# Kernel optimization log

Measured on AMD Instinct MI355X. Metric: run time of the kernel, lower is better.

## Reference

```python
import jax, jax.numpy as jnp
import numpy as np

NV = 100000   # vehicle nodes
NE = 100000   # 'edge' nodes (dst type)
E = 250000    # graph edges (connects relation)
VDIM = 16
EDIM = 16
HID = 128
HEADS = 4
DH = 128      # out_feats per head (GATv2Conv(hid, hid))
EPS = 1e-5
NEG_SLOPE = 0.2


def _layernorm(x, g, b):
    mu = x.mean(-1, keepdims=True)
    var = ((x - mu) ** 2).mean(-1, keepdims=True)
    return (x - mu) * jax.lax.rsqrt(var + EPS) * g + b


def setup_inputs() -> dict:
    key = jax.random.key(0)
    ks = jax.random.split(key, 20)
    s = 0.05
    return {
        "v_feat": jax.random.normal(ks[0], (NV, VDIM), jnp.float32),
        "e_feat": jax.random.normal(ks[1], (NE, EDIM), jnp.float32),
        "Wv": jax.random.normal(ks[2], (VDIM, HID), jnp.float32) * s,
        "bv": jnp.zeros((HID,), jnp.float32),
        "gv": jnp.ones((HID,), jnp.float32),
        "betav": jnp.zeros((HID,), jnp.float32),
        "We": jax.random.normal(ks[3], (EDIM, HID), jnp.float32) * s,
        "be": jnp.zeros((HID,), jnp.float32),
        "ge": jnp.ones((HID,), jnp.float32),
        "betae": jnp.zeros((HID,), jnp.float32),
        "Wsrc": jax.random.normal(ks[4], (HID, HEADS * DH), jnp.float32) * s,
        "bsrc": jnp.zeros((HEADS * DH,), jnp.float32),
        "Wdst": jax.random.normal(ks[5], (HID, HEADS * DH), jnp.float32) * s,
        "bdst": jnp.zeros((HEADS * DH,), jnp.float32),
        "attn": jax.random.normal(ks[6], (HEADS, DH), jnp.float32) * s,
        "Wp": jax.random.normal(ks[7], (HID, HID), jnp.float32) * s,
        "bp": jnp.zeros((HID,), jnp.float32),
        "src": jax.random.randint(ks[8], (E,), 0, NV, jnp.int32),
        "dst": jax.random.randint(ks[9], (E,), 0, NE, jnp.int32),
    }


def reference(v_feat, e_feat, Wv, bv, gv, betav, We, be, ge, betae,
              Wsrc, bsrc, Wdst, bdst, attn, Wp, bp, src, dst):
    # --- node-type encoders: Linear -> ReLU -> LayerNorm ---
    h_v = _layernorm(jax.nn.relu(v_feat @ Wv + bv), gv, betav)      # [NV, HID]
    h_e = _layernorm(jax.nn.relu(e_feat @ We + be), ge, betae)      # [NE, HID]

    # --- GATv2Conv (bipartite: vehicle -> edge), 4 heads ---
    fs = (h_v @ Wsrc + bsrc).reshape(NV, HEADS, DH)                 # src proj
    fd = (h_e @ Wdst + bdst).reshape(NE, HEADS, DH)                 # dst proj
    e = jax.nn.leaky_relu(fs[src] + fd[dst], NEG_SLOPE)             # [E, H, D]
    score = jnp.einsum("ehd,hd->eh", e, attn)                       # [E, H]
    # segment-wise (per-dst-node) softmax over incoming edges
    smax = jax.ops.segment_max(score, dst, num_segments=NE)         # [NE, H]
    ex = jnp.exp(score - smax[dst])
    denom = jax.ops.segment_sum(ex, dst, num_segments=NE)
    alpha = ex / denom[dst]                                         # [E, H]
    out = jax.ops.segment_sum(alpha[:, :, None] * fs[src], dst,
                              num_segments=NE)                      # [NE, H, D]

    # HeteroGraphConv mean-aggregate (single relation -> identity),
    # then mean over heads (edge_out.dim()==3 branch)
    edge_out = out.mean(axis=1)                                     # [NE, HID]

    # feature_proj: Linear -> ReLU -> Dropout(eval: identity)
    return jax.nn.relu(edge_out @ Wp + bp)
```

## Files before the change

### kernel.cpp

```cpp
#include <hip/hip_runtime.h>
#include <hip/hip_bf16.h>
#include <math.h>

#define NV 100000
#define NE_N 100000
#define NEDGE 250000
#define NPAD 100032
#define NEG 0.2f
#define LN_EPS 1e-5f

typedef __bf16 bf16_t;
typedef __bf16 bf16x8 __attribute__((ext_vector_type(8)));
typedef float f32x4 __attribute__((ext_vector_type(4)));
typedef float f32x2 __attribute__((ext_vector_type(2)));

__device__ inline unsigned short f2bfu(float f) {
    return __builtin_bit_cast(unsigned short, (__bf16)f);
}
__device__ inline float blo(unsigned w) { return __uint_as_float(w << 16); }
__device__ inline float bhi(unsigned w) { return __uint_as_float(w & 0xffff0000u); }
__device__ inline float lrelu(float x) { return x > 0.f ? x : NEG * x; }
__device__ inline unsigned pk2(float a, float b) {
    return (unsigned)f2bfu(a) | ((unsigned)f2bfu(b) << 16);
}

__device__ __forceinline__ void gload_lds16(const void* g, void* l) {
    __builtin_amdgcn_global_load_lds(
        (const __attribute__((address_space(1))) unsigned int*)g,
        (__attribute__((address_space(3))) unsigned int*)l,
        16, 0, 0);
}

__global__ __launch_bounds__(256) void prep_kernel(
    const float* __restrict__ Wsrc, const float* __restrict__ Wdst,
    const float* __restrict__ Wp, bf16_t* __restrict__ pS,
    bf16_t* __restrict__ pD, bf16_t* __restrict__ pP,
    int* __restrict__ deg, int* __restrict__ gctr)
{
    int t = blockIdx.x * 256 + threadIdx.x;
    if (t == 0) *gctr = 0;
    if (t < 8192) {
        int ksq = t >> 9, col = t & 511;
#pragma unroll
        for (int j = 0; j < 8; ++j)
            pS[(size_t)t * 8 + j] = (bf16_t)Wsrc[(ksq * 8 + j) * 512 + col];
    } else if (t < 16384) {
        int g = t - 8192;
        int ksq = g >> 9, col = g & 511;
#pragma unroll
        for (int j = 0; j < 8; ++j)
            pD[(size_t)g * 8 + j] = (bf16_t)Wdst[(ksq * 8 + j) * 512 + col];
    } else if (t < 18432) {
        int g = t - 16384;
        int ksq = g >> 7, col = g & 127;
#pragma unroll
        for (int j = 0; j < 8; ++j)
            pP[(size_t)g * 8 + j] = (bf16_t)Wp[(ksq * 8 + j) * 128 + col];
    } else {
        int z = t - 18432;
        if (z < NE_N) deg[z] = 0;
    }
}

__global__ __launch_bounds__(256) void count_kernel(
    const int* __restrict__ dst, int* __restrict__ deg)
{
    int t = blockIdx.x * 256 + threadIdx.x;
    if (t < NEDGE) atomicAdd(&deg[dst[t]], 1);
}

__global__ __launch_bounds__(256) void reserve_kernel(
    const int* __restrict__ deg, int* __restrict__ cursor,
    int2* __restrict__ od, int* __restrict__ gctr)
{
    __shared__ int s[256];
    __shared__ int base;
    int i = blockIdx.x * 256 + threadIdx.x;
    int v = (i < NE_N) ? deg[i] : 0;
    s[threadIdx.x] = v;
    __syncthreads();
    for (int off = 1; off < 256; off <<= 1) {
        int t_ = (threadIdx.x >= off) ? s[threadIdx.x - off] : 0;
        __syncthreads();
        s[threadIdx.x] += t_;
        __syncthreads();
    }
    if (threadIdx.x == 255) base = atomicAdd(gctr, s[255]);
    __syncthreads();
    if (i < NE_N) {
        int o = base + s[threadIdx.x] - v;
        cursor[i] = o;
        od[i] = make_int2(o, v);
    }
}

__global__ __launch_bounds__(256) void scatter_kernel(
    const int* __restrict__ dst, const int* __restrict__ src,
    int* __restrict__ cursor, int* __restrict__ srcs)
{
    int t = blockIdx.x * 256 + threadIdx.x;
    if (t < NEDGE) {
        int pos = atomicAdd(&cursor[dst[t]], 1);
        srcs[pos] = src[t];
    }
}

__global__ __launch_bounds__(256, 4) void enc_proj_kernel(
    const float* __restrict__ featV, const float* __restrict__ WencV,
    const float* __restrict__ bencV, const float* __restrict__ gV,
    const float* __restrict__ betaV, const bf16_t* __restrict__ ApackV,
    const float* __restrict__ bprojV, unsigned short* __restrict__ outV,
    const float* __restrict__ featE, const float* __restrict__ WencE,
    const float* __restrict__ bencE, const float* __restrict__ gE,
    const float* __restrict__ betaE, const bf16_t* __restrict__ ApackE,
    const float* __restrict__ bprojE, unsigned short* __restrict__ outE,
    int nblk1, int M)
{
    __shared__ unsigned short Hs[64 * 136];
    __shared__ __align__(16) unsigned short Abuf[2][8192];
    __shared__ __align__(16) float Bias[512];

    int b = blockIdx.x;
    bool isV = b < nblk1;
    const float* feat  = isV ? featV  : featE;
    const float* Wenc  = isV ? WencV  : WencE;
    const float* benc  = isV ? bencV  : bencE;
    const float* gln   = isV ? gV     : gE;
    const float* beta  = isV ? betaV  : betaE;
    const bf16_t* Apack = isV ? ApackV : ApackE;
    const float* bproj = isV ? bprojV : bprojE;
    unsigned short* out = isV ? outV : outE;
    int row0 = (isV ? b : b - nblk1) * 64;

    int t = threadIdx.x;
    int l = t & 63;
    int w = t >> 6;
    int rbase = __builtin_amdgcn_readfirstlane(w * 16);

    {
        int sr = row0 + rbase + (l >> 2);
        if (sr > M - 1) sr = M - 1;
        gload_lds16(feat + (size_t)sr * 16 + (l & 3) * 4, &Abuf[1][w * 512]);
    }

#pragma unroll
    for (int j = 0; j < 4; ++j) {
        int ksq = w * 4 + j;
        gload_lds16(Apack + ((size_t)(ksq * 512) + l) * 8, &Abuf[0][ksq * 512]);
    }
    if (t < 128)
        *(float4*)&Bias[t * 4] = *(const float4*)(bproj + t * 4);

    f32x2 wc2[16];
#pragma unroll
    for (int k = 0; k < 16; ++k) {
        float2 wv = *(const float2*)(Wenc + k * 128 + 2 * l);
        wc2[k][0] = wv.x;
        wc2[k][1] = wv.y;
    }
    float2 bv2 = *(const float2*)(benc + 2 * l);

    asm volatile("s_waitcnt vmcnt(0)" ::: "memory");

    const float* Fs = (const float*)&Abuf[1][0];
#pragma unroll
    for (int i = 0; i < 16; ++i) {
        const float* fr = Fs + (rbase + i) * 16;
        float4 f0 = *(const float4*)(fr);
        float4 f1 = *(const float4*)(fr + 4);
        float4 f2 = *(const float4*)(fr + 8);
        float4 f3 = *(const float4*)(fr + 12);
        f32x2 a = {bv2.x, bv2.y};
        a = __builtin_elementwise_fma((f32x2)f0.x, wc2[0],  a);
        a = __builtin_elementwise_fma((f32x2)f0.y, wc2[1],  a);
        a = __builtin_elementwise_fma((f32x2)f0.z, wc2[2],  a);
        a = __builtin_elementwise_fma((f32x2)f0.w, wc2[3],  a);
        a = __builtin_elementwise_fma((f32x2)f1.x, wc2[4],  a);
        a = __builtin_elementwise_fma((f32x2)f1.y, wc2[5],  a);
        a = __builtin_elementwise_fma((f32x2)f1.z, wc2[6],  a);
        a = __builtin_elementwise_fma((f32x2)f1.w, wc2[7],  a);
        a = __builtin_elementwise_fma((f32x2)f2.x, wc2[8],  a);
        a = __builtin_elementwise_fma((f32x2)f2.y, wc2[9],  a);
        a = __builtin_elementwise_fma((f32x2)f2.z, wc2[10], a);
        a = __builtin_elementwise_fma((f32x2)f2.w, wc2[11], a);
        a = __builtin_elementwise_fma((f32x2)f3.x, wc2[12], a);
        a = __builtin_elementwise_fma((f32x2)f3.y, wc2[13], a);
        a = __builtin_elementwise_fma((f32x2)f3.z, wc2[14], a);
        a = __builtin_elementwise_fma((f32x2)f3.w, wc2[15], a);
        float a0 = fmaxf(a[0], 0.f);
        float a1 = fmaxf(a[1], 0.f);
        *(unsigned*)&Hs[(rbase + i) * 136 + 2 * l] = pk2(a0, a1);
    }

    float s = 0.f, s2 = 0.f;
    {
        int rr = rbase + (l >> 2);
        int q = l & 3;
#pragma unroll
        for (int j = 0; j < 4; ++j) {
            uint4 v = *(const uint4*)&Hs[rr * 136 + q * 32 + j * 8];
            float x;
            x = blo(v.x); s += x; s2 = fmaf(x, x, s2);
            x = bhi(v.x); s += x; s2 = fmaf(x, x, s2);
            x = blo(v.y); s += x; s2 = fmaf(x, x, s2);
            x = bhi(v.y); s += x; s2 = fmaf(x, x, s2);
            x = blo(v.z); s += x; s2 = fmaf(x, x, s2);
            x = bhi(v.z); s += x; s2 = fmaf(x, x, s2);
            x = blo(v.w); s += x; s2 = fmaf(x, x, s2);
            x = bhi(v.w); s += x; s2 = fmaf(x, x, s2);
        }
    }
    s  += __shfl_xor(s, 1, 64);  s  += __shfl_xor(s, 2, 64);
    s2 += __shfl_xor(s2, 1, 64); s2 += __shfl_xor(s2, 2, 64);
    float mu  = s * (1.f / 128.f);
    float var = s2 * (1.f / 128.f) - mu * mu;
    float inv = rsqrtf(var + LN_EPS);

    int kq = l >> 4;
    int ln = l & 15;
    float mu_r  = __shfl(mu,  ln * 4, 64);
    float inv_r = __shfl(inv, ln * 4, 64);

    bf16x8 bfr[4];
#pragma unroll
    for (int ks = 0; ks < 4; ++ks) {
        int c0 = ks * 32 + kq * 8;
        uint4 v = *(const uint4*)&Hs[(rbase + ln) * 136 + c0];
        float4 g0 = *(const float4*)(gln + c0);
        float4 g1 = *(const float4*)(gln + c0 + 4);
        float4 b0 = *(const float4*)(beta + c0);
        float4 b1 = *(const float4*)(beta + c0 + 4);
        uint4 p;
        p.x = pk2(fmaf((blo(v.x) - mu_r) * inv_r, g0.x, b0.x),
                  fmaf((bhi(v.x) - mu_r) * inv_r, g0.y, b0.y));
        p.y = pk2(fmaf((blo(v.y) - mu_r) * inv_r, g0.z, b0.z),
                  fmaf((bhi(v.y) - mu_r) * inv_r, g0.w, b0.w));
        p.z = pk2(fmaf((blo(v.z) - mu_r) * inv_r, g1.x, b1.x),
                  fmaf((bhi(v.z) - mu_r) * inv_r, g1.y, b1.y));
        p.w = pk2(fmaf((blo(v.w) - mu_r) * inv_r, g1.z, b1.z),
                  fmaf((bhi(v.w) - mu_r) * inv_r, g1.w, b1.w));
        bfr[ks] = __builtin_bit_cast(bf16x8, p);
    }

    unsigned short* stag = Hs + rbase * 136;
    int node = row0 + rbase + ln;

#pragma unroll
    for (int p = 0; p < 8; ++p) {
        if (p == 0)
            asm volatile("s_waitcnt lgkmcnt(0)" ::: "memory");
        else
            asm volatile("s_waitcnt vmcnt(2)" ::: "memory");
        __builtin_amdgcn_s_barrier();

        if (p < 7) {
#pragma unroll
            for (int j = 0; j < 4; ++j) {
                int ksq = w * 4 + j;
                gload_lds16(Apack + ((size_t)(ksq * 512 + (p + 1) * 64) + l) * 8,
                            &Abuf[(p + 1) & 1][ksq * 512]);
            }
            __builtin_amdgcn_sched_barrier(0);
        }

        const unsigned short* Ac = Abuf[p & 1];
#pragma unroll
        for (int mt = 0; mt < 4; ++mt) {
            bf16x8 a[4];
#pragma unroll
            for (int ks = 0; ks < 4; ++ks)
                a[ks] = *(const bf16x8*)&Ac[((ks * 4 + kq) * 64 + mt * 16 + ln) * 8];

            f32x4 acc = {0.f, 0.f, 0.f, 0.f};
#pragma unroll
            for (int ks = 0; ks < 4; ++ks)
                acc = __builtin_amdgcn_mfma_f32_16x16x32_bf16(a[ks], bfr[ks], acc, 0, 0, 0);

            int colp = p * 64 + mt * 16 + kq * 4;
            float4 bb = *(const float4*)&Bias[colp];
            ushort4 o;
            o.x = f2bfu(acc[0] + bb.x);
            o.y = f2bfu(acc[1] + bb.y);
            o.z = f2bfu(acc[2] + bb.z);
            o.w = f2bfu(acc[3] + bb.w);
            *(ushort4*)&stag[ln * 136 + mt * 16 + kq * 4] = o;
        }
#pragma unroll
        for (int i = 0; i < 2; ++i) {
            uint4 v = *(const uint4*)&stag[ln * 136 + i * 32 + kq * 8];
            *(uint4*)(out + (size_t)node * 512 + p * 64 + i * 32 + kq * 8) = v;
        }
    }
}

__global__ __launch_bounds__(256) void final_gemm_kernel(
    const float* __restrict__ A, const unsigned short* __restrict__ Abf,
    const bf16_t* __restrict__ Ppack, const float* __restrict__ bp,
    float* __restrict__ C, int M)
{
    __shared__ unsigned short Hs[64 * 136];
    int t = threadIdx.x;
    int lane = t & 63;
    int w = t >> 6;
    int row0 = blockIdx.x * 64;

    if (Abf) {
#pragma unroll
        for (int i = 0; i < 4; ++i) {
            int idx = i * 256 + t;
            int r = idx >> 4;
            int c = (idx & 15) * 8;
            uint4 v = make_uint4(0, 0, 0, 0);
            if (row0 + r < M)
                v = *(const uint4*)(Abf + (size_t)(row0 + r) * 128 + c);
            *(uint4*)&Hs[r * 136 + c] = v;
        }
    } else {
#pragma unroll
        for (int i = 0; i < 8; ++i) {
            int f4 = i * 256 + t;
            int r = f4 >> 5;
            int c4 = (f4 & 31) * 4;
            float4 v = make_float4(0.f, 0.f, 0.f, 0.f);
            if (row0 + r < M)
                v = ((const float4*)(A + (size_t)(row0 + r) * 128))[f4 & 31];
            ushort4 o;
            o.x = f2bfu(v.x); o.y = f2bfu(v.y); o.z = f2bfu(v.z); o.w = f2bfu(v.w);
            *(ushort4*)&Hs[r * 136 + c4] = o;
        }
    }
    __syncthreads();

    int kq = lane >> 4;
    int ln = lane & 15;

    f32x4 acc[2][4];
#pragma unroll
    for (int mt = 0; mt < 2; ++mt)
#pragma unroll
        for (int nt = 0; nt < 4; ++nt) {
            f32x4 z = {0.f, 0.f, 0.f, 0.f};
            acc[mt][nt] = z;
        }

#pragma unroll
    for (int ks = 0; ks < 4; ++ks) {
        bf16x8 bfr[4];
#pragma unroll
        for (int nt = 0; nt < 4; ++nt) {
            const uint4* p = (const uint4*)&Hs[(nt * 16 + ln) * 136 + ks * 32 + kq * 8];
            bfr[nt] = __builtin_bit_cast(bf16x8, *p);
        }
        bf16x8 afr[2];
#pragma unroll
        for (int mt = 0; mt < 2; ++mt) {
            int colA = w * 32 + mt * 16 + ln;
            afr[mt] = *(const bf16x8*)(Ppack + ((size_t)(ks * 4 + kq) * 128 + colA) * 8);
        }
#pragma unroll
        for (int mt = 0; mt < 2; ++mt)
#pragma unroll
            for (int nt = 0; nt < 4; ++nt)
                acc[mt][nt] = __builtin_amdgcn_mfma_f32_16x16x32_bf16(
                    afr[mt], bfr[nt], acc[mt][nt], 0, 0, 0);
    }

#pragma unroll
    for (int mt = 0; mt < 2; ++mt) {
        int col = w * 32 + mt * 16 + kq * 4;
        float4 bb = *(const float4*)(bp + col);
#pragma unroll
        for (int nt = 0; nt < 4; ++nt) {
            int node = row0 + nt * 16 + ln;
            if (node < M) {
                float4 o;
                o.x = fmaxf(acc[mt][nt][0] + bb.x, 0.f);
                o.y = fmaxf(acc[mt][nt][1] + bb.y, 0.f);
                o.z = fmaxf(acc[mt][nt][2] + bb.z, 0.f);
                o.w = fmaxf(acc[mt][nt][3] + bb.w, 0.f);
                *(float4*)(C + (size_t)node * 128 + col) = o;
            }
        }
    }
}

__global__ __launch_bounds__(256) void softagg_kernel(
    const unsigned short* __restrict__ fs, const unsigned short* __restrict__ fdp,
    const float* __restrict__ attn, const int2* __restrict__ od,
    const int* __restrict__ srcs, float* __restrict__ outf,
    unsigned short* __restrict__ eo)
{
    __shared__ __align__(16) unsigned short Ebuf[4][4][512];
    int wq = threadIdx.x >> 6;
    int d = blockIdx.x * 4 + wq;
    if (d >= NE_N) return;
    int l = threadIdx.x & 63;
    int2 rd = od[d];
    int r0 = rd.x;
    int n  = rd.y;
    int o = l * 8;

    uint4 fv = *(const uint4*)(fdp + (size_t)d * 512 + o);
    float fdv[8] = { blo(fv.x), bhi(fv.x), blo(fv.y), bhi(fv.y),
                     blo(fv.z), bhi(fv.z), blo(fv.w), bhi(fv.w) };
    float4 w0 = *(const float4*)(attn + o);
    float4 w1 = *(const float4*)(attn + o + 4);
    float wv[8] = { w0.x, w0.y, w0.z, w0.w, w1.x, w1.y, w1.z, w1.w };

    float m = -1e30f, sm = 0.f;
    float acc[8];
#pragma unroll
    for (int j = 0; j < 8; ++j) acc[j] = 0.f;

    for (int base = 0; base < n; base += 64) {
        int cnt = min(n - base, 64);
        int sl = 0;
        if (l < cnt) sl = srcs[r0 + base + l];
        for (int c0 = 0; c0 < cnt; c0 += 4) {
            int mc = min(4, cnt - c0);
            for (int j = 0; j < mc; ++j) {
                int s = __shfl(sl, c0 + j, 64);
                gload_lds16(fs + (size_t)s * 512 + l * 8, &Ebuf[wq][j][0]);
            }
            asm volatile("s_waitcnt vmcnt(0)" ::: "memory");
            for (int j = 0; j < mc; ++j) {
                uint4 a = *(const uint4*)&Ebuf[wq][j][o];
                float fsv[8] = { blo(a.x), bhi(a.x), blo(a.y), bhi(a.y),
                                 blo(a.z), bhi(a.z), blo(a.w), bhi(a.w) };
                float p = 0.f;
#pragma unroll
                for (int jj = 0; jj < 8; ++jj)
                    p = fmaf(lrelu(fsv[jj] + fdv[jj]), wv[jj], p);
#pragma unroll
                for (int mk = 1; mk < 16; mk <<= 1)
                    p += __shfl_xor(p, mk, 64);
                float mn = fmaxf(m, p);
                float c  = __expf(m - mn);
                float av = __expf(p - mn);
                sm = sm * c + av;
                m = mn;
#pragma unroll
                for (int jj = 0; jj < 8; ++jj)
                    acc[jj] = fmaf(av, fsv[jj], acc[jj] * c);
            }
        }
    }

    float inv = (n > 0) ? 0.25f / sm : 0.f;
#pragma unroll
    for (int j = 0; j < 8; ++j) {
        float v = acc[j] * inv;
        v += __shfl_xor(v, 16, 64);
        v += __shfl_xor(v, 32, 64);
        acc[j] = v;
    }
    if (l < 16) {
        if (eo) {
            uint4 pk;
            pk.x = pk2(acc[0], acc[1]);
            pk.y = pk2(acc[2], acc[3]);
            pk.z = pk2(acc[4], acc[5]);
            pk.w = pk2(acc[6], acc[7]);
            *(uint4*)(eo + (size_t)d * 128 + l * 8) = pk;
        } else {
            float4 o0 = make_float4(acc[0], acc[1], acc[2], acc[3]);
            float4 o1 = make_float4(acc[4], acc[5], acc[6], acc[7]);
            *(float4*)(outf + (size_t)d * 128 + l * 8) = o0;
            *(float4*)(outf + (size_t)d * 128 + l * 8 + 4) = o1;
        }
    }
}

extern "C" void kernel_launch(void* const* d_in, const int* in_sizes, int n_in,
                              void* d_out, int out_size, void* d_ws, size_t ws_size,
                              hipStream_t stream)
{
    const float* v_feat = (const float*)d_in[0];
    const float* e_feat = (const float*)d_in[1];
    const float* Wv     = (const float*)d_in[2];
    const float* bv     = (const float*)d_in[3];
    const float* gv     = (const float*)d_in[4];
    const float* betav  = (const float*)d_in[5];
    const float* We     = (const float*)d_in[6];
    const float* be     = (const float*)d_in[7];
    const float* ge     = (const float*)d_in[8];
    const float* betae  = (const float*)d_in[9];
    const float* Wsrc   = (const float*)d_in[10];
    const float* bsrc   = (const float*)d_in[11];
    const float* Wdst   = (const float*)d_in[12];
    const float* bdst   = (const float*)d_in[13];
    const float* attn   = (const float*)d_in[14];
    const float* Wp     = (const float*)d_in[15];
    const float* bp     = (const float*)d_in[16];
    const int*   src    = (const int*)d_in[17];
    const int*   dst    = (const int*)d_in[18];
    float* out = (float*)d_out;

    unsigned short* fs = (unsigned short*)d_ws;
    unsigned short* fd = fs + (size_t)NPAD * 512;
    int* deg    = (int*)(fd + (size_t)NPAD * 512);
    int* cursor = deg + NE_N;
    int* gctr   = cursor + NE_N;
    int2* od    = (int2*)(gctr + 4);
    int* srcs   = (int*)(od + NE_N);
    bf16_t* pS  = (bf16_t*)(srcs + NEDGE);
    bf16_t* pD  = pS + 65536;
    bf16_t* pP  = pD + 65536;
    unsigned short* eo = (unsigned short*)(pP + 16384);

    size_t need = (size_t)((char*)(eo + (size_t)NE_N * 128) - (char*)d_ws);
    if (ws_size < need) eo = nullptr;

    const int NB_SCAN = (NE_N + 255) / 256;

    prep_kernel<<<463, 256, 0, stream>>>(Wsrc, Wdst, Wp, pS, pD, pP, deg, gctr);

    count_kernel<<<(NEDGE + 255) / 256, 256, 0, stream>>>(dst, deg);
    reserve_kernel<<<NB_SCAN, 256, 0, stream>>>(deg, cursor, od, gctr);
    scatter_kernel<<<(NEDGE + 255) / 256, 256, 0, stream>>>(dst, src, cursor, srcs);

    enc_proj_kernel<<<3126, 256, 0, stream>>>(
        v_feat, Wv, bv, gv, betav, pS, bsrc, fs,
        e_feat, We, be, ge, betae, pD, bdst, fd,
        1563, 100000);

    softagg_kernel<<<NE_N / 4, 256, 0, stream>>>(fs, fd, attn, od, srcs,
                                                 out, eo);

    final_gemm_kernel<<<1563, 256, 0, stream>>>(out, eo, pP, bp, out, NE_N);
}
```

Baseline: 296.4 us.

## Replace async LDS loads with register loads in projection and aggregation kernels

The projection kernel drops its double-buffered direct global-to-LDS weight staging. It now prefetches the next weight slice into registers and writes it to a single LDS buffer between two block barriers, and the input features get their own small LDS buffer. The softmax-aggregation kernel removes its per-wave LDS staging of gathered source rows and loads each neighbor row directly into registers, one edge at a time. This removes LDS round trips and waitcnt stalls, but it adds extra barriers to the GEMM loop and loses the batching of four outstanding gathers per step in the aggregation.

```diff
diff --git a/kernel.cpp b/kernel.cpp
--- a/kernel.cpp
+++ b/kernel.cpp
@@ -117,7 +117,8 @@
     int nblk1, int M)
 {
     __shared__ unsigned short Hs[64 * 136];
-    __shared__ __align__(16) unsigned short Abuf[2][8192];
+    __shared__ __align__(16) unsigned short Abuf[8192];
+    __shared__ __align__(16) unsigned short Fbuf[2048];
     __shared__ __align__(16) float Bias[512];
 
     int b = blockIdx.x;
@@ -140,13 +141,13 @@
     {
         int sr = row0 + rbase + (l >> 2);
         if (sr > M - 1) sr = M - 1;
-        gload_lds16(feat + (size_t)sr * 16 + (l & 3) * 4, &Abuf[1][w * 512]);
+        gload_lds16(feat + (size_t)sr * 16 + (l & 3) * 4, &Fbuf[w * 512]);
     }
 
 #pragma unroll
     for (int j = 0; j < 4; ++j) {
         int ksq = w * 4 + j;
-        gload_lds16(Apack + ((size_t)(ksq * 512) + l) * 8, &Abuf[0][ksq * 512]);
+        gload_lds16(Apack + ((size_t)(ksq * 512) + l) * 8, &Abuf[ksq * 512]);
     }
     if (t < 128)
         *(float4*)&Bias[t * 4] = *(const float4*)(bproj + t * 4);
@@ -162,7 +163,7 @@
 
     asm volatile("s_waitcnt vmcnt(0)" ::: "memory");
 
-    const float* Fs = (const float*)&Abuf[1][0];
+    const float* Fs = (const float*)&Fbuf[0];
 #pragma unroll
     for (int i = 0; i < 16; ++i) {
         const float* fr = Fs + (rbase + i) * 16;
@@ -242,34 +243,30 @@
         bfr[ks] = __builtin_bit_cast(bf16x8, p);
     }
 
+    __syncthreads();
+
     unsigned short* stag = Hs + rbase * 136;
     int node = row0 + rbase + ln;
 
 #pragma unroll
     for (int p = 0; p < 8; ++p) {
-        if (p == 0)
-            asm volatile("s_waitcnt lgkmcnt(0)" ::: "memory");
-        else
-            asm volatile("s_waitcnt vmcnt(2)" ::: "memory");
-        __builtin_amdgcn_s_barrier();
-
+        uint4 pr[4];
         if (p < 7) {
 #pragma unroll
             for (int j = 0; j < 4; ++j) {
                 int ksq = w * 4 + j;
-                gload_lds16(Apack + ((size_t)(ksq * 512 + (p + 1) * 64) + l) * 8,
-                            &Abuf[(p + 1) & 1][ksq * 512]);
+                pr[j] = *(const uint4*)(Apack +
+                    ((size_t)(ksq * 512 + (p + 1) * 64) + l) * 8);
             }
             __builtin_amdgcn_sched_barrier(0);
         }
 
-        const unsigned short* Ac = Abuf[p & 1];
 #pragma unroll
         for (int mt = 0; mt < 4; ++mt) {
             bf16x8 a[4];
 #pragma unroll
             for (int ks = 0; ks < 4; ++ks)
-                a[ks] = *(const bf16x8*)&Ac[((ks * 4 + kq) * 64 + mt * 16 + ln) * 8];
+                a[ks] = *(const bf16x8*)&Abuf[((ks * 4 + kq) * 64 + mt * 16 + ln) * 8];
 
             f32x4 acc = {0.f, 0.f, 0.f, 0.f};
 #pragma unroll
@@ -289,6 +286,16 @@
         for (int i = 0; i < 2; ++i) {
             uint4 v = *(const uint4*)&stag[ln * 136 + i * 32 + kq * 8];
             *(uint4*)(out + (size_t)node * 512 + p * 64 + i * 32 + kq * 8) = v;
+        }
+
+        if (p < 7) {
+            __syncthreads();
+#pragma unroll
+            for (int j = 0; j < 4; ++j) {
+                int ksq = w * 4 + j;
+                *(uint4*)&Abuf[ksq * 512 + l * 8] = pr[j];
+            }
+            __syncthreads();
         }
     }
 }
@@ -390,9 +397,7 @@
     const int* __restrict__ srcs, float* __restrict__ outf,
     unsigned short* __restrict__ eo)
 {
-    __shared__ __align__(16) unsigned short Ebuf[4][4][512];
-    int wq = threadIdx.x >> 6;
-    int d = blockIdx.x * 4 + wq;
+    int d = blockIdx.x * 4 + (threadIdx.x >> 6);
     if (d >= NE_N) return;
     int l = threadIdx.x & 63;
     int2 rd = od[d];
@@ -416,33 +421,26 @@
         int cnt = min(n - base, 64);
         int sl = 0;
         if (l < cnt) sl = srcs[r0 + base + l];
-        for (int c0 = 0; c0 < cnt; c0 += 4) {
-            int mc = min(4, cnt - c0);
-            for (int j = 0; j < mc; ++j) {
-                int s = __shfl(sl, c0 + j, 64);
-                gload_lds16(fs + (size_t)s * 512 + l * 8, &Ebuf[wq][j][0]);
-            }
-            asm volatile("s_waitcnt vmcnt(0)" ::: "memory");
-            for (int j = 0; j < mc; ++j) {
-                uint4 a = *(const uint4*)&Ebuf[wq][j][o];
-                float fsv[8] = { blo(a.x), bhi(a.x), blo(a.y), bhi(a.y),
-                                 blo(a.z), bhi(a.z), blo(a.w), bhi(a.w) };
-                float p = 0.f;
-#pragma unroll
-                for (int jj = 0; jj < 8; ++jj)
-                    p = fmaf(lrelu(fsv[jj] + fdv[jj]), wv[jj], p);
-#pragma unroll
-                for (int mk = 1; mk < 16; mk <<= 1)
-                    p += __shfl_xor(p, mk, 64);
-                float mn = fmaxf(m, p);
-                float c  = __expf(m - mn);
-                float av = __expf(p - mn);
-                sm = sm * c + av;
-                m = mn;
-#pragma unroll
-                for (int jj = 0; jj < 8; ++jj)
-                    acc[jj] = fmaf(av, fsv[jj], acc[jj] * c);
-            }
+        for (int i = 0; i < cnt; ++i) {
+            int s = __shfl(sl, i, 64);
+            uint4 a = *(const uint4*)(fs + (size_t)s * 512 + o);
+            float fsv[8] = { blo(a.x), bhi(a.x), blo(a.y), bhi(a.y),
+                             blo(a.z), bhi(a.z), blo(a.w), bhi(a.w) };
+            float p = 0.f;
+#pragma unroll
+            for (int j = 0; j < 8; ++j)
+                p = fmaf(lrelu(fsv[j] + fdv[j]), wv[j], p);
+#pragma unroll
+            for (int mk = 1; mk < 16; mk <<= 1)
+                p += __shfl_xor(p, mk, 64);
+            float mn = fmaxf(m, p);
+            float c  = __expf(m - mn);
+            float av = __expf(p - mn);
+            sm = sm * c + av;
+            m = mn;
+#pragma unroll
+            for (int j = 0; j < 8; ++j)
+                acc[j] = fmaf(av, fsv[j], acc[j] * c);
         }
     }
 
```

Result: slower. 364.5 us (+23.0%).
